# Optimization experiments

Hardware: AMD Instinct MI355X
Metric: run time of the kernel (lower is better)

The kernel has to match this reference:

```python
import jax, jax.numpy as jnp
import numpy as np


def setup_inputs() -> dict:
    key = jax.random.key(0)
    k1, k2 = jax.random.split(key)
    batch, n = 1024, 32768
    x = jax.random.normal(k1, (batch, 1, n), dtype=jnp.float32)
    activ = jax.random.uniform(k2, (1, n), dtype=jnp.float32)  # EMA buffer state (nonnegative like mean(|x|))
    std = jnp.ones((1,), dtype=jnp.float32)
    return {"x": x, "activ": activ, "std": std}


def reference(x, activ, std):
    batch = x.shape[0]
    # EMA buffer update: activ = 0.97*activ + 0.03*mean(|x|, axis=0)
    activ_new = 0.97 * activ + 0.03 * jnp.mean(jnp.abs(x), axis=0)  # [1, n]
    ac = jnp.exp(-5.0 * jnp.squeeze(activ_new))                      # [n]
    s = jnp.sum(ac)
    ac = ac.at[0].set(s * 4000.0)  # heavily weight index 0 (the "no perturbation" slot)
    # torch.multinomial(ac, batch, replacement=True) == categorical with logits=log(weights)
    r = jax.random.categorical(jax.random.key(42), jnp.log(ac), shape=(batch,))  # [batch] in [0, n)
    i = jnp.arange(batch)
    # x[i, 0, r] += std * (r > 0); (i, r_i) pairs are unique per row so scatter-add == indexed add
    x = x.at[i, 0, r].add(std * (r > 0).astype(x.dtype))
    return x
```

## Files before the change

### kernel.cpp

```cpp
#include <hip/hip_runtime.h>
#include <math.h>

#define NROWS 1024
#define NCOLS 32768
#define NC4   (NCOLS / 4)
#define HCOLS (NCOLS / 2)
#define NB_SCAN 2048
#define NRB   16
#define KCAND 16
#define TH_BITS 0xFFFC0000u
#define T_GUARD 7.9e-5f

typedef float vfloat4 __attribute__((ext_vector_type(4)));

__device__ __forceinline__ void tf_round(unsigned &x0, unsigned &x1, int r) {
    x0 += x1;
    x1 = __builtin_rotateleft32(x1, r);
    x1 ^= x0;
}

__device__ __forceinline__ void threefry2x32_key0_42(unsigned &x0, unsigned &x1) {
    const unsigned k0 = 0u;
    const unsigned k1 = 42u;
    const unsigned k2 = 0x1BD11BDAu ^ k0 ^ k1;
    x0 += k0; x1 += k1;
    tf_round(x0, x1, 13); tf_round(x0, x1, 15); tf_round(x0, x1, 26); tf_round(x0, x1, 6);
    x0 += k1; x1 += k2 + 1u;
    tf_round(x0, x1, 17); tf_round(x0, x1, 29); tf_round(x0, x1, 16); tf_round(x0, x1, 24);
    x0 += k2; x1 += k0 + 2u;
    tf_round(x0, x1, 13); tf_round(x0, x1, 15); tf_round(x0, x1, 26); tf_round(x0, x1, 6);
    x0 += k0; x1 += k1 + 3u;
    tf_round(x0, x1, 17); tf_round(x0, x1, 29); tf_round(x0, x1, 16); tf_round(x0, x1, 24);
    x0 += k1; x1 += k2 + 4u;
    tf_round(x0, x1, 13); tf_round(x0, x1, 15); tf_round(x0, x1, 26); tf_round(x0, x1, 6);
    x0 += k2; x1 += k0 + 5u;
}

__device__ __forceinline__ float bits_to_u(unsigned bits) {
    float u = __uint_as_float((bits >> 9) | 0x3f800000u) - 1.0f;
    return fmaxf(u, 1.17549435e-38f);
}

template<int U>
__device__ __forceinline__ void scan_group(unsigned cbase, int j0,
                                           unsigned* __restrict__ cntb,
                                           uint2* __restrict__ candb) {
    unsigned x0[U], x1[U];
    const unsigned k0 = 0u;
    const unsigned k1 = 42u;
    const unsigned k2 = 0x1BD11BDAu ^ k0 ^ k1;
#pragma unroll
    for (int u = 0; u < U; ++u) {
        x0[u] = 0u;
        x1[u] = cbase + (unsigned)(j0 + u * 192);
    }
#pragma unroll
    for (int u = 0; u < U; ++u) { x0[u] += k0; x1[u] += k1; }
#define TFR(rr) \
    _Pragma("unroll") \
    for (int u = 0; u < U; ++u) { \
        x0[u] += x1[u]; \
        x1[u] = __builtin_rotateleft32(x1[u], rr); \
        x1[u] ^= x0[u]; \
    }
    TFR(13) TFR(15) TFR(26) TFR(6)
#pragma unroll
    for (int u = 0; u < U; ++u) { x0[u] += k1; x1[u] += k2 + 1u; }
    TFR(17) TFR(29) TFR(16) TFR(24)
#pragma unroll
    for (int u = 0; u < U; ++u) { x0[u] += k2; x1[u] += k0 + 2u; }
    TFR(13) TFR(15) TFR(26) TFR(6)
#pragma unroll
    for (int u = 0; u < U; ++u) { x0[u] += k0; x1[u] += k1 + 3u; }
    TFR(17) TFR(29) TFR(16) TFR(24)
#pragma unroll
    for (int u = 0; u < U; ++u) { x0[u] += k1; x1[u] += k2 + 4u; }
    TFR(13) TFR(15) TFR(26) TFR(6)
#pragma unroll
    for (int u = 0; u < U; ++u) { x0[u] += k2; x1[u] += k0 + 5u; }
#undef TFR
    unsigned bits[U];
#pragma unroll
    for (int u = 0; u < U; ++u) bits[u] = x0[u] ^ x1[u];
    unsigned mx = bits[0];
#pragma unroll
    for (int u = 1; u < U; ++u) mx = mx > bits[u] ? mx : bits[u];
    if (__builtin_expect(mx >= TH_BITS, 0)) {
#pragma unroll
        for (int u = 0; u < U; ++u) {
            const int j = j0 + u * 192;
            if (bits[u] >= TH_BITS && j != 0) {
                unsigned pos = atomicAdd(cntb, 1u);
                if (pos < KCAND) candb[pos] = make_uint2((unsigned)j, bits[u]);
            }
        }
    }
}

__global__ __launch_bounds__(256, 8) void kF(
        const float4* __restrict__ x4, float4* __restrict__ out4,
        float4* __restrict__ partial4, unsigned* __restrict__ bits0,
        unsigned* __restrict__ cnt, uint2* __restrict__ cand) {
    const int b    = blockIdx.x;
    const int t    = threadIdx.x;
    const int wid  = t >> 6;
    const int lane = t & 63;

    if (t == 0) cnt[b] = 0;
    __syncthreads();

    const int copy_wid = b & 3;

    if (wid == copy_wid) {
        const int colg = b & 127;
        const int rowg = b >> 7;
        const int j4   = colg * 64 + lane;
        size_t base = (size_t)(rowg * 64) * NC4 + j4;
        float4 acc = make_float4(0.f, 0.f, 0.f, 0.f);
        #pragma unroll 8
        for (int r = 0; r < 64; ++r) {
            float4 v = x4[base];
            vfloat4 nv = { v.x, v.y, v.z, v.w };
            __builtin_nontemporal_store(nv, (vfloat4*)&out4[base]);
            acc.x += fabsf(v.x); acc.y += fabsf(v.y);
            acc.z += fabsf(v.z); acc.w += fabsf(v.w);
            base += NC4;
        }
        partial4[(size_t)rowg * NC4 + j4] = acc;
    } else {
        const int row  = b >> 1, half = b & 1;
        const int swid = wid - (wid > copy_wid ? 1 : 0);
        const int sl   = swid * 64 + lane;
        const unsigned cbase = (unsigned)row * (unsigned)NCOLS;
        const int jbase = half * HCOLS;

        if (half == 0 && sl == 0) {
            unsigned a0 = 0u, a1 = cbase;
            threefry2x32_key0_42(a0, a1);
            bits0[row] = a0 ^ a1;
        }

        unsigned* cntb  = &cnt[b];
        uint2*    candb = &cand[b * KCAND];
        const int j0    = jbase + sl;
        #pragma unroll 1
        for (int g = 0; g < 10; ++g)
            scan_group<8>(cbase, j0 + g * 8 * 192, cntb, candb);
        scan_group<5>(cbase, j0 + 80 * 192, cntb, candb);
        if (sl < 64)
            scan_group<1>(cbase, j0 + 85 * 192, cntb, candb);
    }
}

__global__ __launch_bounds__(256) void k2_weights(
        const float* __restrict__ partial, const float* __restrict__ activ,
        float* __restrict__ w, float* __restrict__ blocksums,
        float* __restrict__ blockmins) {
    const int t = threadIdx.x;
    const int j = blockIdx.x * 256 + t;
    float s = 0.f;
    #pragma unroll
    for (int rb = 0; rb < NRB; ++rb) s += partial[rb * NCOLS + j];
    float m  = s * (1.0f / (float)NROWS);
    float a  = 0.97f * activ[j] + 0.03f * m;
    float ac = expf(-5.0f * a);
    float wj = 1.0f / ac;
    w[j] = wj;
    __shared__ float reds[256];
    __shared__ float redm[256];
    reds[t] = ac;
    redm[t] = (j == 0) ? INFINITY : wj;
    __syncthreads();
    for (int off = 128; off > 0; off >>= 1) {
        if (t < off) {
            reds[t] += reds[t + off];
            redm[t] = fminf(redm[t], redm[t + off]);
        }
        __syncthreads();
    }
    if (t == 0) { blocksums[blockIdx.x] = reds[0]; blockmins[blockIdx.x] = redm[0]; }
}

__global__ __launch_bounds__(64) void k4_resolve(
        const float* __restrict__ w, const float* __restrict__ blocksums,
        const float* __restrict__ blockmins, const unsigned* __restrict__ bits0,
        const unsigned* __restrict__ cnt, const uint2* __restrict__ cand,
        const float* __restrict__ stdp, float* __restrict__ out) {
    const int r = blockIdx.x;
    const int t = threadIdx.x;
    __shared__ float sv[64];
    __shared__ float sm[64];
    __shared__ int   si[64];

    sv[t] = blocksums[t] + blocksums[t + 64];
    sm[t] = fminf(blockmins[t], blockmins[t + 64]);
    __syncthreads();
    for (int off = 32; off > 0; off >>= 1) {
        if (t < off) {
            sv[t] += sv[t + off];
            sm[t] = fminf(sm[t], sm[t + off]);
        }
        __syncthreads();
    }
    const float w0   = 1.0f / (sv[0] * 4000.0f);
    const float wmin = sm[0];

    const float val0 = -__log2f(bits_to_u(bits0[r])) * w0;
    const unsigned c0 = cnt[2 * r];
    const unsigned c1 = cnt[2 * r + 1];
    const bool slow = (c0 > KCAND) || (c1 > KCAND) || !(val0 < T_GUARD * wmin);

    if (!slow) {
        if (t == 0 && (c0 | c1) != 0u) {
            float best = INFINITY;
            int   bi   = 0x7FFFFFFF;
            for (int k = 0; k < (int)c0; ++k) {
                uint2 cd = cand[(2 * r) * KCAND + k];
                float v = -__log2f(bits_to_u(cd.y)) * w[cd.x];
                int   j = (int)cd.x;
                if (v < best || (v == best && j < bi)) { best = v; bi = j; }
            }
            for (int k = 0; k < (int)c1; ++k) {
                uint2 cd = cand[(2 * r + 1) * KCAND + k];
                float v = -__log2f(bits_to_u(cd.y)) * w[cd.x];
                int   j = (int)cd.x;
                if (v < best || (v == best && j < bi)) { best = v; bi = j; }
            }
            if (best < val0 && bi > 0 && bi < NCOLS)
                out[(size_t)r * NCOLS + bi] += stdp[0];
        }
        return;
    }

    const unsigned cbase = (unsigned)r * (unsigned)NCOLS;
    float best = INFINITY;
    int   bi   = 0x7FFFFFFF;
    for (int j = t; j < NCOLS; j += 64) {
        if (j == 0) continue;
        unsigned x0 = 0u, x1 = cbase + (unsigned)j;
        threefry2x32_key0_42(x0, x1);
        float v = -__log2f(bits_to_u(x0 ^ x1)) * w[j];
        if (v < best) { best = v; bi = j; }
    }
    __syncthreads();
    sv[t] = best; si[t] = bi;
    __syncthreads();
    for (int off = 32; off > 0; off >>= 1) {
        if (t < off) {
            float ov = sv[t + off]; int oi = si[t + off];
            if (ov < sv[t] || (ov == sv[t] && oi < si[t])) { sv[t] = ov; si[t] = oi; }
        }
        __syncthreads();
    }
    if (t == 0) {
        if (sv[0] < val0 && si[0] > 0 && si[0] < NCOLS)
            out[(size_t)r * NCOLS + si[0]] += stdp[0];
    }
}

extern "C" void kernel_launch(void* const* d_in, const int* in_sizes, int n_in,
                              void* d_out, int out_size, void* d_ws, size_t ws_size,
                              hipStream_t stream) {
    (void)in_sizes; (void)n_in; (void)out_size; (void)ws_size;
    const float* x     = (const float*)d_in[0];
    const float* activ = (const float*)d_in[1];
    const float* stdp  = (const float*)d_in[2];
    float* out = (float*)d_out;
    char*  ws  = (char*)d_ws;

    float*    partial   = (float*)ws;
    float*    wbuf      = partial + (size_t)NRB * NCOLS;
    float*    blocksums = wbuf + NCOLS;
    float*    blockmins = blocksums + 128;
    unsigned* bits0     = (unsigned*)(blockmins + 128);
    unsigned* cnt       = bits0 + NROWS;
    uint2*    cand      = (uint2*)(cnt + NB_SCAN);

    kF<<<NB_SCAN, 256, 0, stream>>>((const float4*)x, (float4*)out,
                                    (float4*)partial, bits0, cnt, cand);
    k2_weights<<<NCOLS / 256, 256, 0, stream>>>(partial, activ, wbuf,
                                                blocksums, blockmins);
    k4_resolve<<<NROWS, 64, 0, stream>>>(wbuf, blocksums, blockmins, bits0,
                                         cnt, cand, stdp, out);
}
```

Baseline: 255.6 us.

## Split fused copy/scan kernel into separate copy and RNG-scan kernels

Replaces the single kernel, where one wavefront per block did the memory copy and abs-sum while three wavefronts ran the threefry candidate scan, with two kernels launched back to back. One is a pure copy kernel with 512 blocks of four copy wavefronts, and the other is a scan kernel in which all 256 threads hash with stride 256. This removes the intra-block wavefront divergence and gives each phase a uniform work mapping. In exchange, the memory-bound copy and the ALU-bound hashing no longer overlap within one launch, so the two run serially.

New measurement: 335.8 us. 1.31x slower.

```diff
diff --git a/kernel.cpp b/kernel.cpp
--- a/kernel.cpp
+++ b/kernel.cpp
@@ -41,7 +41,7 @@
     return fmaxf(u, 1.17549435e-38f);
 }
 
-template<int U>
+template<int U, int STRIDE>
 __device__ __forceinline__ void scan_group(unsigned cbase, int j0,
                                            unsigned* __restrict__ cntb,
                                            uint2* __restrict__ candb) {
@@ -52,7 +52,7 @@
 #pragma unroll
     for (int u = 0; u < U; ++u) {
         x0[u] = 0u;
-        x1[u] = cbase + (unsigned)(j0 + u * 192);
+        x1[u] = cbase + (unsigned)(j0 + u * STRIDE);
     }
 #pragma unroll
     for (int u = 0; u < U; ++u) { x0[u] += k0; x1[u] += k1; }
@@ -88,7 +88,7 @@
     if (__builtin_expect(mx >= TH_BITS, 0)) {
 #pragma unroll
         for (int u = 0; u < U; ++u) {
-            const int j = j0 + u * 192;
+            const int j = j0 + u * STRIDE;
             if (bits[u] >= TH_BITS && j != 0) {
                 unsigned pos = atomicAdd(cntb, 1u);
                 if (pos < KCAND) candb[pos] = make_uint2((unsigned)j, bits[u]);
@@ -97,59 +97,55 @@
     }
 }
 
-__global__ __launch_bounds__(256, 8) void kF(
+__global__ __launch_bounds__(256, 8) void kScan(
+        unsigned* __restrict__ bits0, unsigned* __restrict__ cnt,
+        uint2* __restrict__ cand) {
+    const int b = blockIdx.x;
+    const int t = threadIdx.x;
+    const int row = b >> 1, half = b & 1;
+
+    if (t == 0) cnt[b] = 0;
+    __syncthreads();
+
+    const unsigned cbase = (unsigned)row * (unsigned)NCOLS;
+    const int jbase = half * HCOLS;
+
+    if (half == 0 && t == 0) {
+        unsigned a0 = 0u, a1 = cbase;
+        threefry2x32_key0_42(a0, a1);
+        bits0[row] = a0 ^ a1;
+    }
+
+    unsigned* cntb  = &cnt[b];
+    uint2*    candb = &cand[b * KCAND];
+    const int j0    = jbase + t;
+    #pragma unroll 1
+    for (int g = 0; g < 8; ++g)
+        scan_group<8, 256>(cbase, j0 + g * 2048, cntb, candb);
+}
+
+__global__ __launch_bounds__(256, 8) void kCopy(
         const float4* __restrict__ x4, float4* __restrict__ out4,
-        float4* __restrict__ partial4, unsigned* __restrict__ bits0,
-        unsigned* __restrict__ cnt, uint2* __restrict__ cand) {
+        float4* __restrict__ partial4) {
     const int b    = blockIdx.x;
     const int t    = threadIdx.x;
-    const int wid  = t >> 6;
+    const int wgid = b * 4 + (t >> 6);
     const int lane = t & 63;
-
-    if (t == 0) cnt[b] = 0;
-    __syncthreads();
-
-    const int copy_wid = b & 3;
-
-    if (wid == copy_wid) {
-        const int colg = b & 127;
-        const int rowg = b >> 7;
-        const int j4   = colg * 64 + lane;
-        size_t base = (size_t)(rowg * 64) * NC4 + j4;
-        float4 acc = make_float4(0.f, 0.f, 0.f, 0.f);
-        #pragma unroll 8
-        for (int r = 0; r < 64; ++r) {
-            float4 v = x4[base];
-            vfloat4 nv = { v.x, v.y, v.z, v.w };
-            __builtin_nontemporal_store(nv, (vfloat4*)&out4[base]);
-            acc.x += fabsf(v.x); acc.y += fabsf(v.y);
-            acc.z += fabsf(v.z); acc.w += fabsf(v.w);
-            base += NC4;
-        }
-        partial4[(size_t)rowg * NC4 + j4] = acc;
-    } else {
-        const int row  = b >> 1, half = b & 1;
-        const int swid = wid - (wid > copy_wid ? 1 : 0);
-        const int sl   = swid * 64 + lane;
-        const unsigned cbase = (unsigned)row * (unsigned)NCOLS;
-        const int jbase = half * HCOLS;
-
-        if (half == 0 && sl == 0) {
-            unsigned a0 = 0u, a1 = cbase;
-            threefry2x32_key0_42(a0, a1);
-            bits0[row] = a0 ^ a1;
-        }
-
-        unsigned* cntb  = &cnt[b];
-        uint2*    candb = &cand[b * KCAND];
-        const int j0    = jbase + sl;
-        #pragma unroll 1
-        for (int g = 0; g < 10; ++g)
-            scan_group<8>(cbase, j0 + g * 8 * 192, cntb, candb);
-        scan_group<5>(cbase, j0 + 80 * 192, cntb, candb);
-        if (sl < 64)
-            scan_group<1>(cbase, j0 + 85 * 192, cntb, candb);
-    }
+    const int colg = wgid & 127;
+    const int rowg = wgid >> 7;
+    const int j4   = colg * 64 + lane;
+    size_t base = (size_t)(rowg * 64) * NC4 + j4;
+    float4 acc = make_float4(0.f, 0.f, 0.f, 0.f);
+    #pragma unroll 8
+    for (int r = 0; r < 64; ++r) {
+        float4 v = x4[base];
+        vfloat4 nv = { v.x, v.y, v.z, v.w };
+        __builtin_nontemporal_store(nv, (vfloat4*)&out4[base]);
+        acc.x += fabsf(v.x); acc.y += fabsf(v.y);
+        acc.z += fabsf(v.z); acc.w += fabsf(v.w);
+        base += NC4;
+    }
+    partial4[(size_t)rowg * NC4 + j4] = acc;
 }
 
 __global__ __launch_bounds__(256) void k2_weights(
@@ -276,8 +272,9 @@
     unsigned* cnt       = bits0 + NROWS;
     uint2*    cand      = (uint2*)(cnt + NB_SCAN);
 
-    kF<<<NB_SCAN, 256, 0, stream>>>((const float4*)x, (float4*)out,
-                                    (float4*)partial, bits0, cnt, cand);
+    kCopy<<<512, 256, 0, stream>>>((const float4*)x, (float4*)out,
+                                   (float4*)partial);
+    kScan<<<NB_SCAN, 256, 0, stream>>>(bits0, cnt, cand);
     k2_weights<<<NCOLS / 256, 256, 0, stream>>>(partial, activ, wbuf,
                                                 blocksums, blockmins);
     k4_resolve<<<NROWS, 64, 0, stream>>>(wbuf, blocksums, blockmins, bits0,
```
